# Performance work log

Hardware: AMD Instinct MI355X
Metric: run time of the kernel (lower is better)

The kernel has to match this reference:

```python
import jax, jax.numpy as jnp
import numpy as np

EMBED_DIM = 1024
NUM_HEADS = 16
HEAD_DIM = EMBED_DIM // NUM_HEADS


def setup_inputs() -> dict:
    key = jax.random.key(0)
    k1, k2, k3 = jax.random.split(key, 3)
    B, T = 2, 2048
    query = jax.random.normal(k1, (B, T, EMBED_DIM), dtype=jnp.float32)
    # xavier_uniform_ for Linear(embed_dim, 3*embed_dim): limit = sqrt(6/(fan_in+fan_out))
    lim_qkv = float(np.sqrt(6.0 / (EMBED_DIM + 3 * EMBED_DIM)))
    Wqkv = jax.random.uniform(k2, (3 * EMBED_DIM, EMBED_DIM), dtype=jnp.float32,
                              minval=-lim_qkv, maxval=lim_qkv)
    bqkv = jnp.zeros((3 * EMBED_DIM,), dtype=jnp.float32)
    lim_o = float(np.sqrt(6.0 / (EMBED_DIM + EMBED_DIM)))
    Wo = jax.random.uniform(k3, (EMBED_DIM, EMBED_DIM), dtype=jnp.float32,
                            minval=-lim_o, maxval=lim_o)
    bo = jnp.zeros((EMBED_DIM,), dtype=jnp.float32)
    return {"query": query, "Wqkv": Wqkv, "bqkv": bqkv, "Wo": Wo, "bo": bo}


def reference(query, Wqkv, bqkv, Wo, bo):
    B, T, E = query.shape
    H, D = NUM_HEADS, HEAD_DIM
    scaling = D ** -0.5
    # fused qkv projection from `query` (original ignores key/value tensors)
    qkv = jnp.einsum('bte,fe->btf', query, Wqkv) + bqkv  # [B, T, 3E]
    q, k, v = jnp.split(qkv, 3, axis=-1)
    # [B, H, T, D]
    q = q.reshape(B, T, H, D).transpose(0, 2, 1, 3) * scaling
    k = k.reshape(B, T, H, D).transpose(0, 2, 1, 3)
    v = v.reshape(B, T, H, D).transpose(0, 2, 1, 3)
    scores = jnp.einsum('bhtd,bhsd->bhts', q, k)          # [B, H, T, T]
    attn = jax.nn.softmax(scores, axis=-1)
    out = jnp.einsum('bhts,bhsd->bhtd', attn, v)           # [B, H, T, D]
    out = out.transpose(0, 2, 1, 3).reshape(B, T, E)
    out = jnp.einsum('bte,fe->btf', out, Wo) + bo
    return out
```

## Files before the change

kernel.cpp:

```cpp
#include <hip/hip_runtime.h>
#include <hip/hip_bf16.h>

#define B_ 2
#define T_ 2048
#define E_ 1024
#define H_ 16
#define D_ 64
#define F_ 3072
#define M_ 4096
#define VT_STRIDE 2080
#define QSCALE 0.1803368801111f
#define THR_LOG2 11.5f

typedef __attribute__((ext_vector_type(8))) short short8v;
typedef __attribute__((ext_vector_type(4))) float float4v;

#if __has_builtin(__builtin_amdgcn_exp2f)
#define EXP2(x) __builtin_amdgcn_exp2f(x)
#else
#define EXP2(x) exp2f(x)
#endif

__device__ __forceinline__ unsigned cvtpk(float lo, float hi) {
    union { __hip_bfloat162 h; unsigned u; } x;
    x.h = __float22bfloat162_rn(float2{lo, hi});
    return x.u;
}
__device__ __forceinline__ ushort f2bf(float f) { return (ushort)cvtpk(f, f); }

__global__ void cvt_kernel(const float* __restrict__ in, ushort* __restrict__ out, int n4) {
    int i = blockIdx.x * blockDim.x + threadIdx.x;
    if (i >= n4) return;
    float4 v = ((const float4*)in)[i];
    uint2 o;
    o.x = cvtpk(v.x, v.y);
    o.y = cvtpk(v.z, v.w);
    ((uint2*)out)[i] = o;
}

template <int MODE>
__global__ __launch_bounds__(256) void gemm_bt(const ushort* __restrict__ A,
                                               const ushort* __restrict__ Bt,
                                               const float* __restrict__ bias,
                                               void* __restrict__ Cout,
                                               int Ndim, int K) {
    __shared__ __attribute__((aligned(16))) char lds[32768];
    int t = threadIdx.x;
    int lane = t & 63;
    int w = t >> 6;
    int wr = w >> 1, wc = w & 1;
    int bm0 = blockIdx.x * 128, bn0 = blockIdx.y * 128;
    int mb = bm0 + wr * 64;
    int nb = bn0 + wc * 64;
    int r15 = lane & 15, g = lane >> 4;

    int srow = w * 8 + (lane >> 3);
    int schunk = (lane & 7) ^ (lane >> 3);
    const ushort* Asrc = A + (size_t)(bm0 + srow) * K + schunk * 8;
    const ushort* Bsrc = Bt + (size_t)(bn0 + srow) * K + schunk * 8;

    int rxor7 = r15 & 7;
    int abase = (wr * 64 + r15) * 128;
    int bbase = 16384 + (wc * 64 + r15) * 128;

    float4v acc[4][4] = {};
    for (int k0 = 0; k0 < K; k0 += 64) {
#pragma unroll
        for (int j = 0; j < 4; ++j) {
            __builtin_amdgcn_global_load_lds(
                (const __attribute__((address_space(1))) void*)(Asrc + (size_t)(j * 32) * K + k0),
                (__attribute__((address_space(3))) void*)(lds + j * 4096 + w * 1024),
                16, 0, 0);
            __builtin_amdgcn_global_load_lds(
                (const __attribute__((address_space(1))) void*)(Bsrc + (size_t)(j * 32) * K + k0),
                (__attribute__((address_space(3))) void*)(lds + 16384 + j * 4096 + w * 1024),
                16, 0, 0);
        }
        __syncthreads();

        short8v af[4][2], bf[4][2];
#pragma unroll
        for (int r = 0; r < 4; ++r)
#pragma unroll
            for (int h = 0; h < 2; ++h)
                af[r][h] = *(const short8v*)(lds + abase + r * 2048 +
                                             (((h * 4 + g) ^ rxor7) << 4));
#pragma unroll
        for (int c = 0; c < 4; ++c)
#pragma unroll
            for (int h = 0; h < 2; ++h)
                bf[c][h] = *(const short8v*)(lds + bbase + c * 2048 +
                                             (((h * 4 + g) ^ rxor7) << 4));
#pragma unroll
        for (int r = 0; r < 4; ++r)
#pragma unroll
            for (int c = 0; c < 4; ++c) {
                acc[r][c] = __builtin_amdgcn_mfma_f32_16x16x32_bf16(af[r][0], bf[c][0], acc[r][c], 0, 0, 0);
                acc[r][c] = __builtin_amdgcn_mfma_f32_16x16x32_bf16(af[r][1], bf[c][1], acc[r][c], 0, 0, 0);
            }
        __syncthreads();
    }

    if (MODE == 0) {
        ushort* qkv = (ushort*)Cout;
#pragma unroll
        for (int r = 0; r < 4; ++r)
#pragma unroll
            for (int c = 0; c < 4; ++c)
#pragma unroll
                for (int ri = 0; ri < 4; ++ri) {
                    int m = mb + r * 16 + g * 4 + ri;
                    int n = nb + c * 16 + r15;
                    float v = acc[r][c][ri] + bias[n];
                    int which = n >> 10;
                    int e = n & 1023;
                    if (which == 0) v *= QSCALE;
                    int h = e >> 6, d = e & 63;
                    int b = m >> 11, tt0 = m & 2047;
                    size_t addr;
                    if (which == 2) {
                        int tt = tt0 & 63;
                        int c64 = ((tt >> 2) & 3) * 16 + (tt >> 4) * 4 + (tt & 3);
                        int tp = (tt0 & ~63) | c64;
                        addr = (size_t)2 * M_ * E_ +
                               ((size_t)(b * H_ + h) * D_ + d) * VT_STRIDE + tp;
                    } else {
                        addr = (size_t)which * M_ * E_ +
                               ((size_t)(b * H_ + h) * T_ + tt0) * D_ + d;
                    }
                    qkv[addr] = f2bf(v);
                }
    } else {
        float* out = (float*)Cout;
#pragma unroll
        for (int r = 0; r < 4; ++r)
#pragma unroll
            for (int c = 0; c < 4; ++c)
#pragma unroll
                for (int ri = 0; ri < 4; ++ri) {
                    int m = mb + r * 16 + g * 4 + ri;
                    int n = nb + c * 16 + r15;
                    out[(size_t)m * Ndim + n] = acc[r][c][ri] + bias[n];
                }
    }
}

__global__ __launch_bounds__(256, 2) void attn_kernel(const ushort* __restrict__ qkv,
                                                      ushort* __restrict__ Ob) {
    __shared__ __attribute__((aligned(16))) char lds[32768];
    int tid = threadIdx.x;
    int lane = tid & 63;
    int w = tid >> 6;
    int bid = blockIdx.x;
    int slot = bid >> 3;
    int bh = (bid & 7) * 4 + (slot >> 4);
    int qt = slot & 15;
    int r15 = lane & 15, g = lane >> 4;
    int qb = qt * 128 + w * 32;

    const ushort* Qh = qkv + (size_t)bh * T_ * D_;
    const ushort* Kh = qkv + (size_t)M_ * E_ + (size_t)bh * T_ * D_;
    const ushort* Vt = qkv + (size_t)2 * M_ * E_ + (size_t)bh * D_ * VT_STRIDE;

    const ushort* QrowA = Qh + (size_t)(qb + r15) * D_ + g * 8;
    short8v qfA0 = *(const short8v*)(QrowA);
    short8v qfA1 = *(const short8v*)(QrowA + 32);
    short8v qfB0 = *(const short8v*)(QrowA + 16 * D_);
    short8v qfB1 = *(const short8v*)(QrowA + 16 * D_ + 32);
    asm volatile("" :: "v"(qfA0), "v"(qfA1), "v"(qfB0), "v"(qfB1));

    float4v oaccA[4] = {}, oaccB[4] = {};
    float mA = -1e30f, lA = 0.f;
    float mB = -1e30f, lB = 0.f;

    int srow = tid >> 3;
    int slc = (tid & 7) ^ (srow & 7);
    const ushort* Ksrc = Kh + (size_t)srow * D_ + slc * 8;
    const ushort* Vsrc = Vt + (size_t)srow * VT_STRIDE + slc * 8;

    auto stage = [&](int kt, int base) {
        const ushort* kp = Ksrc + (size_t)kt * 64 * D_;
        const ushort* vp = Vsrc + kt * 64;
#pragma unroll
        for (int i = 0; i < 2; ++i)
            __builtin_amdgcn_global_load_lds(
                (const __attribute__((address_space(1))) void*)(kp + (size_t)i * 32 * D_),
                (__attribute__((address_space(3))) void*)(lds + base + i * 4096 + tid * 16),
                16, 0, 0);
#pragma unroll
        for (int i = 0; i < 2; ++i)
            __builtin_amdgcn_global_load_lds(
                (const __attribute__((address_space(1))) void*)(vp + (size_t)i * 32 * VT_STRIDE),
                (__attribute__((address_space(3))) void*)(lds + base + 8192 + i * 4096 + tid * 16),
                16, 0, 0);
    };

    int rxor = (r15 & 7) << 4;
    int rowb = r15 * 128;
    int kc0 = ((g) << 4) ^ rxor;
    int kc1 = ((g + 4) << 4) ^ rxor;
    int vc0 = ((2 * g) << 4) ^ rxor;
    int vc1 = ((2 * g + 1) << 4) ^ rxor;

    auto softmax64 = [&](const float4v& s0, const float4v& s1, const float4v& s2,
                         const float4v& s3, float& m_run, float& l_run,
                         float4v* oacc, short8v& pf0, short8v& pf1) {
        float t0 = fmaxf(fmaxf(s0[0], s0[1]), fmaxf(s0[2], s0[3]));
        float t1 = fmaxf(fmaxf(s1[0], s1[1]), fmaxf(s1[2], s1[3]));
        float t2 = fmaxf(fmaxf(s2[0], s2[1]), fmaxf(s2[2], s2[3]));
        float t3 = fmaxf(fmaxf(s3[0], s3[1]), fmaxf(s3[2], s3[3]));
        float tmax = fmaxf(fmaxf(t0, t1), fmaxf(t2, t3));
        if (!__all(tmax - m_run <= THR_LOG2)) {
            float tr = fmaxf(tmax, __shfl_xor(tmax, 16));
            tr = fmaxf(tr, __shfl_xor(tr, 32));
            float mnew = fmaxf(m_run, tr);
            float corr = EXP2(m_run - mnew);
            float c0 = __shfl(corr, g * 4 + 0);
            float c1 = __shfl(corr, g * 4 + 1);
            float c2 = __shfl(corr, g * 4 + 2);
            float c3 = __shfl(corr, g * 4 + 3);
#pragma unroll
            for (int c = 0; c < 4; ++c) {
                oacc[c][0] *= c0; oacc[c][1] *= c1;
                oacc[c][2] *= c2; oacc[c][3] *= c3;
            }
            l_run *= corr;
            m_run = mnew;
        }
        float p0 = EXP2(s0[0] - m_run), p1 = EXP2(s0[1] - m_run);
        float p2 = EXP2(s0[2] - m_run), p3 = EXP2(s0[3] - m_run);
        float p4 = EXP2(s1[0] - m_run), p5 = EXP2(s1[1] - m_run);
        float p6 = EXP2(s1[2] - m_run), p7 = EXP2(s1[3] - m_run);
        float p8 = EXP2(s2[0] - m_run), p9 = EXP2(s2[1] - m_run);
        float pa = EXP2(s2[2] - m_run), pb = EXP2(s2[3] - m_run);
        float pc = EXP2(s3[0] - m_run), pd = EXP2(s3[1] - m_run);
        float pe = EXP2(s3[2] - m_run), pg = EXP2(s3[3] - m_run);
        l_run += (((p0 + p1) + (p2 + p3)) + ((p4 + p5) + (p6 + p7))) +
                 (((p8 + p9) + (pa + pb)) + ((pc + pd) + (pe + pg)));
        union { short8v v; unsigned u[4]; } u0, u1;
        u0.u[0] = cvtpk(p0, p1); u0.u[1] = cvtpk(p2, p3);
        u0.u[2] = cvtpk(p4, p5); u0.u[3] = cvtpk(p6, p7);
        u1.u[0] = cvtpk(p8, p9); u1.u[1] = cvtpk(pa, pb);
        u1.u[2] = cvtpk(pc, pd); u1.u[3] = cvtpk(pe, pg);
        pf0 = u0.v; pf1 = u1.v;
    };

    auto compute = [&](int base) {
        const char* kb_ = lds + base;
        const char* vb_ = lds + base + 8192;
        short8v k0a = *(const short8v*)(kb_ + rowb + kc0);
        short8v k0b = *(const short8v*)(kb_ + rowb + kc1);
        short8v k1a = *(const short8v*)(kb_ + 2048 + rowb + kc0);
        short8v k1b = *(const short8v*)(kb_ + 2048 + rowb + kc1);
        short8v k2a = *(const short8v*)(kb_ + 4096 + rowb + kc0);
        short8v k2b = *(const short8v*)(kb_ + 4096 + rowb + kc1);
        short8v k3a = *(const short8v*)(kb_ + 6144 + rowb + kc0);
        short8v k3b = *(const short8v*)(kb_ + 6144 + rowb + kc1);

        float4v sA0 = {}, sA1 = {}, sA2 = {}, sA3 = {};
        float4v sB0 = {}, sB1 = {}, sB2 = {}, sB3 = {};
        __builtin_amdgcn_s_setprio(1);
        sA0 = __builtin_amdgcn_mfma_f32_16x16x32_bf16(k0a, qfA0, sA0, 0, 0, 0);
        sA0 = __builtin_amdgcn_mfma_f32_16x16x32_bf16(k0b, qfA1, sA0, 0, 0, 0);
        sA1 = __builtin_amdgcn_mfma_f32_16x16x32_bf16(k1a, qfA0, sA1, 0, 0, 0);
        sA1 = __builtin_amdgcn_mfma_f32_16x16x32_bf16(k1b, qfA1, sA1, 0, 0, 0);
        sA2 = __builtin_amdgcn_mfma_f32_16x16x32_bf16(k2a, qfA0, sA2, 0, 0, 0);
        sA2 = __builtin_amdgcn_mfma_f32_16x16x32_bf16(k2b, qfA1, sA2, 0, 0, 0);
        sA3 = __builtin_amdgcn_mfma_f32_16x16x32_bf16(k3a, qfA0, sA3, 0, 0, 0);
        sA3 = __builtin_amdgcn_mfma_f32_16x16x32_bf16(k3b, qfA1, sA3, 0, 0, 0);
        sB0 = __builtin_amdgcn_mfma_f32_16x16x32_bf16(k0a, qfB0, sB0, 0, 0, 0);
        sB0 = __builtin_amdgcn_mfma_f32_16x16x32_bf16(k0b, qfB1, sB0, 0, 0, 0);
        sB1 = __builtin_amdgcn_mfma_f32_16x16x32_bf16(k1a, qfB0, sB1, 0, 0, 0);
        sB1 = __builtin_amdgcn_mfma_f32_16x16x32_bf16(k1b, qfB1, sB1, 0, 0, 0);
        sB2 = __builtin_amdgcn_mfma_f32_16x16x32_bf16(k2a, qfB0, sB2, 0, 0, 0);
        sB2 = __builtin_amdgcn_mfma_f32_16x16x32_bf16(k2b, qfB1, sB2, 0, 0, 0);
        sB3 = __builtin_amdgcn_mfma_f32_16x16x32_bf16(k3a, qfB0, sB3, 0, 0, 0);
        sB3 = __builtin_amdgcn_mfma_f32_16x16x32_bf16(k3b, qfB1, sB3, 0, 0, 0);
        __builtin_amdgcn_s_setprio(0);

        short8v v0a = *(const short8v*)(vb_ + rowb + vc0);
        short8v v0b = *(const short8v*)(vb_ + rowb + vc1);
        short8v v1a = *(const short8v*)(vb_ + 2048 + rowb + vc0);
        short8v v1b = *(const short8v*)(vb_ + 2048 + rowb + vc1);
        short8v v2a = *(const short8v*)(vb_ + 4096 + rowb + vc0);
        short8v v2b = *(const short8v*)(vb_ + 4096 + rowb + vc1);
        short8v v3a = *(const short8v*)(vb_ + 6144 + rowb + vc0);
        short8v v3b = *(const short8v*)(vb_ + 6144 + rowb + vc1);

        short8v pA0, pA1, pB0, pB1;
        softmax64(sA0, sA1, sA2, sA3, mA, lA, oaccA, pA0, pA1);
        softmax64(sB0, sB1, sB2, sB3, mB, lB, oaccB, pB0, pB1);

        __builtin_amdgcn_s_setprio(1);
        oaccA[0] = __builtin_amdgcn_mfma_f32_16x16x32_bf16(pA0, v0a, oaccA[0], 0, 0, 0);
        oaccA[0] = __builtin_amdgcn_mfma_f32_16x16x32_bf16(pA1, v0b, oaccA[0], 0, 0, 0);
        oaccB[0] = __builtin_amdgcn_mfma_f32_16x16x32_bf16(pB0, v0a, oaccB[0], 0, 0, 0);
        oaccB[0] = __builtin_amdgcn_mfma_f32_16x16x32_bf16(pB1, v0b, oaccB[0], 0, 0, 0);
        oaccA[1] = __builtin_amdgcn_mfma_f32_16x16x32_bf16(pA0, v1a, oaccA[1], 0, 0, 0);
        oaccA[1] = __builtin_amdgcn_mfma_f32_16x16x32_bf16(pA1, v1b, oaccA[1], 0, 0, 0);
        oaccB[1] = __builtin_amdgcn_mfma_f32_16x16x32_bf16(pB0, v1a, oaccB[1], 0, 0, 0);
        oaccB[1] = __builtin_amdgcn_mfma_f32_16x16x32_bf16(pB1, v1b, oaccB[1], 0, 0, 0);
        oaccA[2] = __builtin_amdgcn_mfma_f32_16x16x32_bf16(pA0, v2a, oaccA[2], 0, 0, 0);
        oaccA[2] = __builtin_amdgcn_mfma_f32_16x16x32_bf16(pA1, v2b, oaccA[2], 0, 0, 0);
        oaccB[2] = __builtin_amdgcn_mfma_f32_16x16x32_bf16(pB0, v2a, oaccB[2], 0, 0, 0);
        oaccB[2] = __builtin_amdgcn_mfma_f32_16x16x32_bf16(pB1, v2b, oaccB[2], 0, 0, 0);
        oaccA[3] = __builtin_amdgcn_mfma_f32_16x16x32_bf16(pA0, v3a, oaccA[3], 0, 0, 0);
        oaccA[3] = __builtin_amdgcn_mfma_f32_16x16x32_bf16(pA1, v3b, oaccA[3], 0, 0, 0);
        oaccB[3] = __builtin_amdgcn_mfma_f32_16x16x32_bf16(pB0, v3a, oaccB[3], 0, 0, 0);
        oaccB[3] = __builtin_amdgcn_mfma_f32_16x16x32_bf16(pB1, v3b, oaccB[3], 0, 0, 0);
        __builtin_amdgcn_s_setprio(0);
    };

    stage(0, 0);
    for (int kt = 0; kt < T_ / 64; kt += 2) {
        stage(kt + 1, 16384);
        asm volatile("s_waitcnt vmcnt(4)" ::: "memory");
        __builtin_amdgcn_s_barrier();
        compute(0);
        __builtin_amdgcn_s_barrier();
        if (kt + 2 < T_ / 64) {
            stage(kt + 2, 0);
            asm volatile("s_waitcnt vmcnt(4)" ::: "memory");
        } else {
            asm volatile("s_waitcnt vmcnt(0)" ::: "memory");
        }
        __builtin_amdgcn_s_barrier();
        compute(16384);
        __builtin_amdgcn_s_barrier();
    }

    lA += __shfl_xor(lA, 16); lA += __shfl_xor(lA, 32);
    lB += __shfl_xor(lB, 16); lB += __shfl_xor(lB, 32);

    int b = bh >> 4, h = bh & 15;
    {
        float i0 = 1.f / __shfl(lA, g * 4 + 0), i1 = 1.f / __shfl(lA, g * 4 + 1);
        float i2 = 1.f / __shfl(lA, g * 4 + 2), i3 = 1.f / __shfl(lA, g * 4 + 3);
#pragma unroll
        for (int c = 0; c < 4; ++c) {
            size_t base = ((size_t)b * T_ + qb + g * 4) * E_ + h * 64 + c * 16 + r15;
            Ob[base]          = f2bf(oaccA[c][0] * i0);
            Ob[base + E_]     = f2bf(oaccA[c][1] * i1);
            Ob[base + 2 * E_] = f2bf(oaccA[c][2] * i2);
            Ob[base + 3 * E_] = f2bf(oaccA[c][3] * i3);
        }
    }
    {
        float i0 = 1.f / __shfl(lB, g * 4 + 0), i1 = 1.f / __shfl(lB, g * 4 + 1);
        float i2 = 1.f / __shfl(lB, g * 4 + 2), i3 = 1.f / __shfl(lB, g * 4 + 3);
#pragma unroll
        for (int c = 0; c < 4; ++c) {
            size_t base = ((size_t)b * T_ + qb + 16 + g * 4) * E_ + h * 64 + c * 16 + r15;
            Ob[base]          = f2bf(oaccB[c][0] * i0);
            Ob[base + E_]     = f2bf(oaccB[c][1] * i1);
            Ob[base + 2 * E_] = f2bf(oaccB[c][2] * i2);
            Ob[base + 3 * E_] = f2bf(oaccB[c][3] * i3);
        }
    }
}

extern "C" void kernel_launch(void* const* d_in, const int* in_sizes, int n_in,
                              void* d_out, int out_size, void* d_ws, size_t ws_size,
                              hipStream_t stream) {
    const float* query = (const float*)d_in[0];
    const float* Wqkv  = (const float*)d_in[1];
    const float* bqkv  = (const float*)d_in[2];
    const float* Wo    = (const float*)d_in[3];
    const float* bo    = (const float*)d_in[4];
    float* out = (float*)d_out;

    ushort* Xb    = (ushort*)d_ws;
    ushort* Wqkvb = Xb + (size_t)M_ * E_;
    ushort* Wob   = Wqkvb + (size_t)F_ * E_;
    ushort* QKVb  = Wob + (size_t)E_ * E_;
    ushort* Ob    = Xb;

    cvt_kernel<<<(M_ * E_ / 4 + 255) / 256, 256, 0, stream>>>(query, Xb, M_ * E_ / 4);
    cvt_kernel<<<(F_ * E_ / 4 + 255) / 256, 256, 0, stream>>>(Wqkv, Wqkvb, F_ * E_ / 4);
    cvt_kernel<<<(E_ * E_ / 4 + 255) / 256, 256, 0, stream>>>(Wo, Wob, E_ * E_ / 4);

    gemm_bt<0><<<dim3(M_ / 128, F_ / 128), 256, 0, stream>>>(Xb, Wqkvb, bqkv, QKVb, F_, E_);
    attn_kernel<<<(B_ * H_) * (T_ / 128), 256, 0, stream>>>(QKVb, Ob);
    gemm_bt<1><<<dim3(M_ / 128, E_ / 128), 256, 0, stream>>>(Ob, Wob, bo, out, E_, E_);
}
```

Baseline: 197.1 us.

## Split attention KV range across two wave groups and merge softmax states

The attention kernel now launches 512 threads per block, with two groups of four waves. Each group processes half of every 128-key stage for the same query rows, and the two partial online-softmax states are merged through LDS at the end. This doubles the waves available to hide latency per query tile, at the cost of twice the LDS (64KB), an extra merge pass and launch bounds that may pressure registers. The QKV GEMM epilogue is also restructured to hoist per-column bias and scale and to write V-transposed outputs as vectorized 4-element stores.

```diff
diff --git a/kernel.cpp b/kernel.cpp
--- a/kernel.cpp
+++ b/kernel.cpp
@@ -20,6 +20,9 @@
 #else
 #define EXP2(x) exp2f(x)
 #endif
+
+#define AS1 const __attribute__((address_space(1))) void*
+#define AS3 __attribute__((address_space(3))) void*
 
 __device__ __forceinline__ unsigned cvtpk(float lo, float hi) {
     union { __hip_bfloat162 h; unsigned u; } x;
@@ -68,13 +71,11 @@
 #pragma unroll
         for (int j = 0; j < 4; ++j) {
             __builtin_amdgcn_global_load_lds(
-                (const __attribute__((address_space(1))) void*)(Asrc + (size_t)(j * 32) * K + k0),
-                (__attribute__((address_space(3))) void*)(lds + j * 4096 + w * 1024),
-                16, 0, 0);
+                (AS1)(Asrc + (size_t)(j * 32) * K + k0),
+                (AS3)(lds + j * 4096 + w * 1024), 16, 0, 0);
             __builtin_amdgcn_global_load_lds(
-                (const __attribute__((address_space(1))) void*)(Bsrc + (size_t)(j * 32) * K + k0),
-                (__attribute__((address_space(3))) void*)(lds + 16384 + j * 4096 + w * 1024),
-                16, 0, 0);
+                (AS1)(Bsrc + (size_t)(j * 32) * K + k0),
+                (AS3)(lds + 16384 + j * 4096 + w * 1024), 16, 0, 0);
         }
         __syncthreads();
 
@@ -106,30 +107,39 @@
 #pragma unroll
         for (int r = 0; r < 4; ++r)
 #pragma unroll
-            for (int c = 0; c < 4; ++c)
-#pragma unroll
-                for (int ri = 0; ri < 4; ++ri) {
-                    int m = mb + r * 16 + g * 4 + ri;
-                    int n = nb + c * 16 + r15;
-                    float v = acc[r][c][ri] + bias[n];
-                    int which = n >> 10;
-                    int e = n & 1023;
-                    if (which == 0) v *= QSCALE;
-                    int h = e >> 6, d = e & 63;
-                    int b = m >> 11, tt0 = m & 2047;
-                    size_t addr;
-                    if (which == 2) {
-                        int tt = tt0 & 63;
-                        int c64 = ((tt >> 2) & 3) * 16 + (tt >> 4) * 4 + (tt & 3);
-                        int tp = (tt0 & ~63) | c64;
-                        addr = (size_t)2 * M_ * E_ +
-                               ((size_t)(b * H_ + h) * D_ + d) * VT_STRIDE + tp;
-                    } else {
-                        addr = (size_t)which * M_ * E_ +
-                               ((size_t)(b * H_ + h) * T_ + tt0) * D_ + d;
+            for (int c = 0; c < 4; ++c) {
+                int n0 = nb + c * 16;
+                int which = n0 >> 10;
+                int n = n0 + r15;
+                int e = n & 1023;
+                int h = e >> 6, d = e & 63;
+                int m0 = mb + r * 16 + g * 4;
+                int b = m0 >> 11, t0 = m0 & 2047;
+                if (which == 2) {
+                    int tt = t0 & 63;
+                    int c64 = ((tt >> 2) & 3) * 16 + (tt >> 4) * 4 + (tt & 3);
+                    size_t addr = (size_t)2 * M_ * E_ +
+                                  ((size_t)(b * H_ + h) * D_ + d) * VT_STRIDE +
+                                  ((t0 & ~63) | c64);
+                    float bv = bias[n];
+                    ushort4 o;
+                    o.x = f2bf(acc[r][c][0] + bv);
+                    o.y = f2bf(acc[r][c][1] + bv);
+                    o.z = f2bf(acc[r][c][2] + bv);
+                    o.w = f2bf(acc[r][c][3] + bv);
+                    *(ushort4*)(qkv + addr) = o;
+                } else {
+                    float bv = bias[n];
+                    float sc = (which == 0) ? QSCALE : 1.0f;
+#pragma unroll
+                    for (int ri = 0; ri < 4; ++ri) {
+                        float v = (acc[r][c][ri] + bv) * sc;
+                        size_t addr = (size_t)which * M_ * E_ +
+                                      ((size_t)(b * H_ + h) * T_ + t0 + ri) * D_ + d;
+                        qkv[addr] = f2bf(v);
                     }
-                    qkv[addr] = f2bf(v);
                 }
+            }
     } else {
         float* out = (float*)Cout;
 #pragma unroll
@@ -145,18 +155,20 @@
     }
 }
 
-__global__ __launch_bounds__(256, 2) void attn_kernel(const ushort* __restrict__ qkv,
+__global__ __launch_bounds__(512, 4) void attn_kernel(const ushort* __restrict__ qkv,
                                                       ushort* __restrict__ Ob) {
-    __shared__ __attribute__((aligned(16))) char lds[32768];
+    __shared__ __attribute__((aligned(16))) char lds[65536];
     int tid = threadIdx.x;
     int lane = tid & 63;
     int w = tid >> 6;
+    int gid = w >> 2;
+    int wp = w & 3;
     int bid = blockIdx.x;
     int slot = bid >> 3;
     int bh = (bid & 7) * 4 + (slot >> 4);
     int qt = slot & 15;
     int r15 = lane & 15, g = lane >> 4;
-    int qb = qt * 128 + w * 32;
+    int qb = qt * 128 + wp * 32;
 
     const ushort* Qh = qkv + (size_t)bh * T_ * D_;
     const ushort* Kh = qkv + (size_t)M_ * E_ + (size_t)bh * T_ * D_;
@@ -173,34 +185,32 @@
     float mA = -1e30f, lA = 0.f;
     float mB = -1e30f, lB = 0.f;
 
-    int srow = tid >> 3;
-    int slc = (tid & 7) ^ (srow & 7);
-    const ushort* Ksrc = Kh + (size_t)srow * D_ + slc * 8;
-    const ushort* Vsrc = Vt + (size_t)srow * VT_STRIDE + slc * 8;
-
-    auto stage = [&](int kt, int base) {
-        const ushort* kp = Ksrc + (size_t)kt * 64 * D_;
-        const ushort* vp = Vsrc + kt * 64;
-#pragma unroll
-        for (int i = 0; i < 2; ++i)
-            __builtin_amdgcn_global_load_lds(
-                (const __attribute__((address_space(1))) void*)(kp + (size_t)i * 32 * D_),
-                (__attribute__((address_space(3))) void*)(lds + base + i * 4096 + tid * 16),
-                16, 0, 0);
-#pragma unroll
-        for (int i = 0; i < 2; ++i)
-            __builtin_amdgcn_global_load_lds(
-                (const __attribute__((address_space(1))) void*)(vp + (size_t)i * 32 * VT_STRIDE),
-                (__attribute__((address_space(3))) void*)(lds + base + 8192 + i * 4096 + tid * 16),
-                16, 0, 0);
+    int srowK = tid >> 3;
+    int slcK = (tid & 7) ^ (srowK & 7);
+    const ushort* Ksrc = Kh + (size_t)srowK * D_ + slcK * 8;
+    int srowV = tid >> 4;
+    int slcV = (tid & 15) ^ (srowV & 15);
+    const ushort* Vsrc = Vt + (size_t)srowV * VT_STRIDE + slcV * 8;
+
+    auto stage = [&](int st, int base) {
+        const ushort* kp = Ksrc + (size_t)st * 128 * D_;
+        const ushort* vp = Vsrc + st * 128;
+        __builtin_amdgcn_global_load_lds((AS1)kp, (AS3)(lds + base + tid * 16), 16, 0, 0);
+        __builtin_amdgcn_global_load_lds((AS1)(kp + (size_t)64 * D_),
+                                         (AS3)(lds + base + 8192 + tid * 16), 16, 0, 0);
+        __builtin_amdgcn_global_load_lds((AS1)vp, (AS3)(lds + base + 16384 + tid * 16), 16, 0, 0);
+        __builtin_amdgcn_global_load_lds((AS1)(vp + (size_t)32 * VT_STRIDE),
+                                         (AS3)(lds + base + 24576 + tid * 16), 16, 0, 0);
     };
 
     int rxor = (r15 & 7) << 4;
     int rowb = r15 * 128;
-    int kc0 = ((g) << 4) ^ rxor;
+    int kbg = gid * 8192;
+    int kc0 = (g << 4) ^ rxor;
     int kc1 = ((g + 4) << 4) ^ rxor;
-    int vc0 = ((2 * g) << 4) ^ rxor;
-    int vc1 = ((2 * g + 1) << 4) ^ rxor;
+    int vrow = r15 * 256;
+    int vc0 = ((gid * 8 + 2 * g) ^ r15) << 4;
+    int vc1 = ((gid * 8 + 2 * g + 1) ^ r15) << 4;
 
     auto softmax64 = [&](const float4v& s0, const float4v& s1, const float4v& s2,
                          const float4v& s3, float& m_run, float& l_run,
@@ -246,8 +256,8 @@
     };
 
     auto compute = [&](int base) {
-        const char* kb_ = lds + base;
-        const char* vb_ = lds + base + 8192;
+        const char* kb_ = lds + base + kbg;
+        const char* vb_ = lds + base + 16384;
         short8v k0a = *(const short8v*)(kb_ + rowb + kc0);
         short8v k0b = *(const short8v*)(kb_ + rowb + kc1);
         short8v k1a = *(const short8v*)(kb_ + 2048 + rowb + kc0);
@@ -278,14 +288,14 @@
         sB3 = __builtin_amdgcn_mfma_f32_16x16x32_bf16(k3b, qfB1, sB3, 0, 0, 0);
         __builtin_amdgcn_s_setprio(0);
 
-        short8v v0a = *(const short8v*)(vb_ + rowb + vc0);
-        short8v v0b = *(const short8v*)(vb_ + rowb + vc1);
-        short8v v1a = *(const short8v*)(vb_ + 2048 + rowb + vc0);
-        short8v v1b = *(const short8v*)(vb_ + 2048 + rowb + vc1);
-        short8v v2a = *(const short8v*)(vb_ + 4096 + rowb + vc0);
-        short8v v2b = *(const short8v*)(vb_ + 4096 + rowb + vc1);
-        short8v v3a = *(const short8v*)(vb_ + 6144 + rowb + vc0);
-        short8v v3b = *(const short8v*)(vb_ + 6144 + rowb + vc1);
+        short8v v0a = *(const short8v*)(vb_ + vrow + vc0);
+        short8v v0b = *(const short8v*)(vb_ + vrow + vc1);
+        short8v v1a = *(const short8v*)(vb_ + 4096 + vrow + vc0);
+        short8v v1b = *(const short8v*)(vb_ + 4096 + vrow + vc1);
+        short8v v2a = *(const short8v*)(vb_ + 8192 + vrow + vc0);
+        short8v v2b = *(const short8v*)(vb_ + 8192 + vrow + vc1);
+        short8v v3a = *(const short8v*)(vb_ + 12288 + vrow + vc0);
+        short8v v3b = *(const short8v*)(vb_ + 12288 + vrow + vc1);
 
         short8v pA0, pA1, pB0, pB1;
         softmax64(sA0, sA1, sA2, sA3, mA, lA, oaccA, pA0, pA1);
@@ -312,49 +322,83 @@
     };
 
     stage(0, 0);
-    for (int kt = 0; kt < T_ / 64; kt += 2) {
-        stage(kt + 1, 16384);
+    for (int st = 0; st < T_ / 128; st += 2) {
+        stage(st + 1, 32768);
         asm volatile("s_waitcnt vmcnt(4)" ::: "memory");
         __builtin_amdgcn_s_barrier();
         compute(0);
         __builtin_amdgcn_s_barrier();
-        if (kt + 2 < T_ / 64) {
-            stage(kt + 2, 0);
+        if (st + 2 < T_ / 128) {
+            stage(st + 2, 0);
             asm volatile("s_waitcnt vmcnt(4)" ::: "memory");
         } else {
             asm volatile("s_waitcnt vmcnt(0)" ::: "memory");
         }
         __builtin_amdgcn_s_barrier();
-        compute(16384);
+        compute(32768);
         __builtin_amdgcn_s_barrier();
     }
 
     lA += __shfl_xor(lA, 16); lA += __shfl_xor(lA, 32);
     lB += __shfl_xor(lB, 16); lB += __shfl_xor(lB, 32);
-
-    int b = bh >> 4, h = bh & 15;
-    {
-        float i0 = 1.f / __shfl(lA, g * 4 + 0), i1 = 1.f / __shfl(lA, g * 4 + 1);
-        float i2 = 1.f / __shfl(lA, g * 4 + 2), i3 = 1.f / __shfl(lA, g * 4 + 3);
-#pragma unroll
-        for (int c = 0; c < 4; ++c) {
-            size_t base = ((size_t)b * T_ + qb + g * 4) * E_ + h * 64 + c * 16 + r15;
-            Ob[base]          = f2bf(oaccA[c][0] * i0);
-            Ob[base + E_]     = f2bf(oaccA[c][1] * i1);
-            Ob[base + 2 * E_] = f2bf(oaccA[c][2] * i2);
-            Ob[base + 3 * E_] = f2bf(oaccA[c][3] * i3);
-        }
+    __syncthreads();
+    float* mf = (float*)lds;
+    int reg = wp * 2176;
+    if (gid == 1) {
+        if (lane < 16) {
+            mf[reg + lane] = mA;      mf[reg + 16 + lane] = lA;
+            mf[reg + 32 + lane] = mB; mf[reg + 48 + lane] = lB;
+        }
+#pragma unroll
+        for (int c = 0; c < 4; ++c)
+#pragma unroll
+            for (int ri = 0; ri < 4; ++ri) {
+                mf[reg + 64 + (g * 4 + ri) * 64 + c * 16 + r15] = oaccA[c][ri];
+                mf[reg + 1088 + (g * 4 + ri) * 64 + c * 16 + r15] = oaccB[c][ri];
+            }
     }
-    {
-        float i0 = 1.f / __shfl(lB, g * 4 + 0), i1 = 1.f / __shfl(lB, g * 4 + 1);
-        float i2 = 1.f / __shfl(lB, g * 4 + 2), i3 = 1.f / __shfl(lB, g * 4 + 3);
-#pragma unroll
-        for (int c = 0; c < 4; ++c) {
-            size_t base = ((size_t)b * T_ + qb + 16 + g * 4) * E_ + h * 64 + c * 16 + r15;
-            Ob[base]          = f2bf(oaccB[c][0] * i0);
-            Ob[base + E_]     = f2bf(oaccB[c][1] * i1);
-            Ob[base + 2 * E_] = f2bf(oaccB[c][2] * i2);
-            Ob[base + 3 * E_] = f2bf(oaccB[c][3] * i3);
+    __syncthreads();
+    if (gid == 0) {
+        int b = bh >> 4, h = bh & 15;
+        {
+            float mh = mf[reg + r15], lh = mf[reg + 16 + r15];
+            float mM = fmaxf(mA, mh);
+            float ca = EXP2(mA - mM), cb = EXP2(mh - mM);
+            float inv = 1.f / (ca * lA + cb * lh);
+            float af = ca * inv, bfx = cb * inv;
+            float a0 = __shfl(af, g * 4 + 0), b0 = __shfl(bfx, g * 4 + 0);
+            float a1 = __shfl(af, g * 4 + 1), b1 = __shfl(bfx, g * 4 + 1);
+            float a2 = __shfl(af, g * 4 + 2), b2 = __shfl(bfx, g * 4 + 2);
+            float a3 = __shfl(af, g * 4 + 3), b3 = __shfl(bfx, g * 4 + 3);
+#pragma unroll
+            for (int c = 0; c < 4; ++c) {
+                size_t base = ((size_t)b * T_ + qb + g * 4) * E_ + h * 64 + c * 16 + r15;
+                int lb = reg + 64 + g * 4 * 64 + c * 16 + r15;
+                Ob[base]          = f2bf(a0 * oaccA[c][0] + b0 * mf[lb]);
+                Ob[base + E_]     = f2bf(a1 * oaccA[c][1] + b1 * mf[lb + 64]);
+                Ob[base + 2 * E_] = f2bf(a2 * oaccA[c][2] + b2 * mf[lb + 128]);
+                Ob[base + 3 * E_] = f2bf(a3 * oaccA[c][3] + b3 * mf[lb + 192]);
+            }
+        }
+        {
+            float mh = mf[reg + 32 + r15], lh = mf[reg + 48 + r15];
+            float mM = fmaxf(mB, mh);
+            float ca = EXP2(mB - mM), cb = EXP2(mh - mM);
+            float inv = 1.f / (ca * lB + cb * lh);
+            float af = ca * inv, bfx = cb * inv;
+            float a0 = __shfl(af, g * 4 + 0), b0 = __shfl(bfx, g * 4 + 0);
+            float a1 = __shfl(af, g * 4 + 1), b1 = __shfl(bfx, g * 4 + 1);
+            float a2 = __shfl(af, g * 4 + 2), b2 = __shfl(bfx, g * 4 + 2);
+            float a3 = __shfl(af, g * 4 + 3), b3 = __shfl(bfx, g * 4 + 3);
+#pragma unroll
+            for (int c = 0; c < 4; ++c) {
+                size_t base = ((size_t)b * T_ + qb + 16 + g * 4) * E_ + h * 64 + c * 16 + r15;
+                int lb = reg + 1088 + g * 4 * 64 + c * 16 + r15;
+                Ob[base]          = f2bf(a0 * oaccB[c][0] + b0 * mf[lb]);
+                Ob[base + E_]     = f2bf(a1 * oaccB[c][1] + b1 * mf[lb + 64]);
+                Ob[base + 2 * E_] = f2bf(a2 * oaccB[c][2] + b2 * mf[lb + 128]);
+                Ob[base + 3 * E_] = f2bf(a3 * oaccB[c][3] + b3 * mf[lb + 192]);
+            }
         }
     }
 }
@@ -380,6 +424,6 @@
     cvt_kernel<<<(E_ * E_ / 4 + 255) / 256, 256, 0, stream>>>(Wo, Wob, E_ * E_ / 4);
 
     gemm_bt<0><<<dim3(M_ / 128, F_ / 128), 256, 0, stream>>>(Xb, Wqkvb, bqkv, QKVb, F_, E_);
-    attn_kernel<<<(B_ * H_) * (T_ / 128), 256, 0, stream>>>(QKVb, Ob);
+    attn_kernel<<<(B_ * H_) * (T_ / 128), 512, 0, stream>>>(QKVb, Ob);
     gemm_bt<1><<<dim3(M_ / 128, E_ / 128), 256, 0, stream>>>(Ob, Wob, bo, out, E_, E_);
 }
```

Measured after the change: 253.5 us. +28.6%, slower.
